# Kernel optimization log

Hardware: AMD Instinct MI355X
Metric: run time of the kernel (lower is better)

## Reference

```python
import jax, jax.numpy as jnp
import numpy as np

N_NODES = 100_000
N_EDGES = 1_600_000
N_GRAPHS = 1_000
NODES_PER_GRAPH = 100
N_NODE_FEATS = 64
DIM_STATE = 32
DIM_OUT = 64
DIM_NODE_EMB = 64
HID = 128
HEADS = 8
BASES = 4


def _lin(key, out_f, in_f, bias=True):
    k1, k2 = jax.random.split(key)
    lim = 1.0 / np.sqrt(in_f)
    w = jax.random.uniform(k1, (out_f, in_f), minval=-lim, maxval=lim, dtype=jnp.float32)
    if not bias:
        return w
    b = jax.random.uniform(k2, (out_f,), minval=-lim, maxval=lim, dtype=jnp.float32)
    return w, b


def setup_inputs() -> dict:
    key = jax.random.key(0)
    ks = jax.random.split(key, 16)
    x = jax.random.normal(ks[0], (N_NODES, N_NODE_FEATS), dtype=jnp.float32)
    edge_index = jax.random.randint(ks[1], (2, N_EDGES), 0, N_NODES, dtype=jnp.int32)
    batch = jnp.arange(N_NODES, dtype=jnp.int32) // NODES_PER_GRAPH  # sorted segment ids
    n_atoms = jnp.full((N_GRAPHS, 1), NODES_PER_GRAPH, dtype=jnp.int32)  # consistent with batch
    z_e = jax.random.normal(ks[2], (N_GRAPHS, DIM_STATE), dtype=jnp.float32)
    nfc_w, nfc_b = _lin(ks[3], HID, N_NODE_FEATS)
    # EGConv: bases Linear(in, (out//heads)*bases, no bias); comb Linear(in, heads*bases); bias (out,)
    gc1_bases_w = _lin(ks[4], (HID // HEADS) * BASES, HID, bias=False)
    gc1_comb_w, gc1_comb_b = _lin(ks[5], HEADS * BASES, HID)
    gc1_bias = jnp.zeros((HID,), jnp.float32)
    gc2_bases_w = _lin(ks[6], (DIM_NODE_EMB // HEADS) * BASES, HID, bias=False)
    gc2_comb_w, gc2_comb_b = _lin(ks[7], HEADS * BASES, HID)
    gc2_bias = jnp.zeros((DIM_NODE_EMB,), jnp.float32)
    attn_w, attn_b = _lin(ks[8], 1, DIM_NODE_EMB + DIM_STATE)
    fcg_w, fcg_b = _lin(ks[9], DIM_OUT, DIM_NODE_EMB)
    fccg_w, fccg_b = _lin(ks[10], DIM_OUT, DIM_NODE_EMB)
    return {"x": x, "edge_index": edge_index, "batch": batch, "n_atoms": n_atoms, "z_e": z_e,
            "nfc_w": nfc_w, "nfc_b": nfc_b,
            "gc1_bases_w": gc1_bases_w, "gc1_comb_w": gc1_comb_w, "gc1_comb_b": gc1_comb_b, "gc1_bias": gc1_bias,
            "gc2_bases_w": gc2_bases_w, "gc2_comb_w": gc2_comb_w, "gc2_comb_b": gc2_comb_b, "gc2_bias": gc2_bias,
            "attn_w": attn_w, "attn_b": attn_b, "fcg_w": fcg_w, "fcg_b": fcg_b, "fccg_w": fccg_w, "fccg_b": fccg_b}


def _egconv(h, src, dst, bases_w, comb_w, comb_b, bias, heads=HEADS, nbases=BASES):
    # PyG EGConv with aggregators=['symnorm'], add_self_loops=True
    n = h.shape[0]
    out_ch = bias.shape[0]
    deg = jnp.ones((n,), h.dtype).at[dst].add(1.0)          # in-degree + self loop
    dis = jax.lax.rsqrt(deg)                                 # deg^-1/2
    b = h @ bases_w.T                                        # [n, nbases*(out_ch//heads)]
    # symnorm aggregation incl. self-loop term dis_i^2 * b_i
    agg = ((dis * dis)[:, None] * b).at[dst].add((dis[src] * dis[dst])[:, None] * b[src])
    w = (h @ comb_w.T + comb_b).reshape(n, heads, nbases)    # [n, H, B]
    agg = agg.reshape(n, nbases, out_ch // heads)            # [n, B, F/H]
    return jnp.einsum('nhb,nbf->nhf', w, agg).reshape(n, out_ch) + bias


def reference(x, edge_index, batch, n_atoms, z_e, nfc_w, nfc_b,
              gc1_bases_w, gc1_comb_w, gc1_comb_b, gc1_bias,
              gc2_bases_w, gc2_comb_w, gc2_comb_b, gc2_bias,
              attn_w, attn_b, fcg_w, fcg_b, fccg_w, fccg_b):
    src, dst = edge_index[0], edge_index[1]
    h = jax.nn.elu(x @ nfc_w.T + nfc_b)
    h = jax.nn.elu(_egconv(h, src, dst, gc1_bases_w, gc1_comb_w, gc1_comb_b, gc1_bias))
    h = jax.nn.elu(_egconv(h, src, dst, gc2_bases_w, gc2_comb_w, gc2_comb_b, gc2_bias))
    h = h / jnp.maximum(jnp.linalg.norm(h, axis=1, keepdims=True), 1e-12)  # L2 normalize
    z_a = jax.ops.segment_sum(h, batch, num_segments=N_GRAPHS) @ fcg_w.T + fcg_b
    z_rep = jnp.repeat(z_e, n_atoms[:, 0], axis=0, total_repeat_length=N_NODES)
    logits = jnp.concatenate([h, z_rep], axis=1) @ attn_w.T + attn_b + 1e-16  # [N,1]
    m = jax.ops.segment_max(logits, batch, num_segments=N_GRAPHS)
    e = jnp.exp(logits - m[batch])
    denom = jax.ops.segment_sum(e, batch, num_segments=N_GRAPHS) + 1e-16
    attns = e / denom[batch]
    z_c = jax.ops.segment_sum(attns * h, batch, num_segments=N_GRAPHS) @ fccg_w.T + fccg_b
    return z_a, z_c, h
```

## Files before the change

### kernel.cpp

```cpp
#include <hip/hip_runtime.h>
#include <hip/hip_bf16.h>
#include <math.h>

#define N_NODES  100000
#define N_EDGES  1600000
#define N_GRAPHS 1000
#define NPG      100
#define NBKT     391
#define BCAP     5120
#define EPB      16384
#define NBE      ((N_EDGES + EPB - 1) / EPB)
#define GBA      ((N_NODES + 63) / 64)

typedef float  f32x4 __attribute__((ext_vector_type(4)));
typedef short  s16x8 __attribute__((ext_vector_type(8)));

__device__ __forceinline__ float elu_f(float x) {
    return x > 0.0f ? x : expm1f(x);
}
__device__ __forceinline__ float bf2f(unsigned int u16) {
    union { unsigned int i; float f; } v; v.i = u16 << 16; return v.f;
}
__device__ __forceinline__ unsigned short f2bf(float f) {
    __hip_bfloat16 h = __float2bfloat16(f);
    return *reinterpret_cast<unsigned short*>(&h);
}
__device__ __forceinline__ s16x8 cvt8(const float4& a, const float4& b) {
    s16x8 o;
    o[0]=(short)f2bf(a.x); o[1]=(short)f2bf(a.y); o[2]=(short)f2bf(a.z); o[3]=(short)f2bf(a.w);
    o[4]=(short)f2bf(b.x); o[5]=(short)f2bf(b.y); o[6]=(short)f2bf(b.z); o[7]=(short)f2bf(b.w);
    return o;
}

__global__ __launch_bounds__(512) void setup_k(
    int* __restrict__ bkt_cur,
    const float* __restrict__ w0, const float* __restrict__ w1c, const float* __restrict__ w1w,
    const float* __restrict__ w2c, const float* __restrict__ w2w, unsigned short* __restrict__ wb)
{
    int t = threadIdx.x;
    if (blockIdx.x == 0 && t < NBKT) bkt_cur[t] = t * BCAP;
    int i = blockIdx.x * 512 + t;
    float v;
    if (i < 8192)       v = w0[i];
    else if (i < 16384) v = w1c[i - 8192];
    else if (i < 20480) v = w1w[i - 16384];
    else if (i < 24576) v = w2c[i - 20480];
    else if (i < 28672) v = w2w[i - 24576];
    else return;
    wb[i] = f2bf(v);
}

__global__ __launch_bounds__(256) void scatterA_k(
    const float* __restrict__ x, const unsigned short* __restrict__ wb,
    const float* __restrict__ b0, const float* __restrict__ bw,
    unsigned short* __restrict__ c1out, float* __restrict__ w1out, int M,
    const int* __restrict__ ei, int* __restrict__ bkt_cur, unsigned int* __restrict__ pairs)
{
    __shared__ union {
        struct { int h[NBKT]; int base[NBKT]; } sc;
        unsigned short hT[64][136];
    } u;

    const int t = threadIdx.x;

    if (blockIdx.x < NBE) {
        const int eb = blockIdx.x;
        int* h = u.sc.h;
        int* base = u.sc.base;
        for (int i = t; i < NBKT; i += 256) h[i] = 0;
        __syncthreads();
        const int4* src4 = (const int4*)ei;
        const int4* dst4 = (const int4*)(ei + N_EDGES);
        int i0 = eb * (EPB / 4);
        for (int i = t; i < EPB / 4; i += 256) {
            int g = i0 + i;
            if (g < N_EDGES / 4) {
                int4 d = dst4[g];
                atomicAdd(&h[d.x >> 8], 1);
                atomicAdd(&h[d.y >> 8], 1);
                atomicAdd(&h[d.z >> 8], 1);
                atomicAdd(&h[d.w >> 8], 1);
            }
        }
        __syncthreads();
        for (int i = t; i < NBKT; i += 256) {
            int c = h[i];
            base[i] = c ? atomicAdd(&bkt_cur[i], c) : 0;
            h[i] = 0;
        }
        __syncthreads();
        for (int i = t; i < EPB / 4; i += 256) {
            int g = i0 + i;
            if (g < N_EDGES / 4) {
                int4 s4 = src4[g];
                int4 d4 = dst4[g];
                int b, r;
                b = d4.x >> 8; r = atomicAdd(&h[b], 1); pairs[base[b] + r] = ((unsigned)s4.x << 8) | (d4.x & 255);
                b = d4.y >> 8; r = atomicAdd(&h[b], 1); pairs[base[b] + r] = ((unsigned)s4.y << 8) | (d4.y & 255);
                b = d4.z >> 8; r = atomicAdd(&h[b], 1); pairs[base[b] + r] = ((unsigned)s4.z << 8) | (d4.z & 255);
                b = d4.w >> 8; r = atomicAdd(&h[b], 1); pairs[base[b] + r] = ((unsigned)s4.w << 8) | (d4.w & 255);
            }
        }
        return;
    }

    const unsigned short* W0b = wb;
    const unsigned short* Wcb = wb + 8192;
    const unsigned short* Wwb = wb + 16384;

    const int wave = t >> 6, lane = t & 63;
    const int lr = lane & 15, lk = lane >> 4;
    const int blockRow = (blockIdx.x - NBE) * 64;

    {
        const int wr = wave >> 1, wc = wave & 1;
        f32x4 acc[2][4];
        #pragma unroll
        for (int rt = 0; rt < 2; ++rt)
            #pragma unroll
            for (int ct = 0; ct < 4; ++ct) acc[rt][ct] = (f32x4){0.f,0.f,0.f,0.f};

        #pragma unroll
        for (int kt = 0; kt < 2; ++kt) {
            const int k0 = kt * 32 + lk * 8;
            s16x8 afr[2];
            #pragma unroll
            for (int rt = 0; rt < 2; ++rt) {
                int r = blockRow + (wr * 2 + rt) * 16 + lr;
                r = (r < M) ? r : (M - 1);
                const float* ap = x + (size_t)r * 64 + k0;
                afr[rt] = cvt8(*(const float4*)ap, *(const float4*)(ap + 4));
            }
            s16x8 bfr[4];
            #pragma unroll
            for (int ct = 0; ct < 4; ++ct) {
                int n = (wc * 4 + ct) * 16 + lr;
                bfr[ct] = *(const s16x8*)(W0b + (size_t)n * 64 + k0);
            }
            #pragma unroll
            for (int rt = 0; rt < 2; ++rt)
                #pragma unroll
                for (int ct = 0; ct < 4; ++ct)
                    acc[rt][ct] = __builtin_amdgcn_mfma_f32_16x16x32_bf16(afr[rt], bfr[ct], acc[rt][ct], 0, 0, 0);
        }
        #pragma unroll
        for (int rt = 0; rt < 2; ++rt) {
            int lmb = (wr * 2 + rt) * 16 + lk * 4;
            #pragma unroll
            for (int j = 0; j < 4; ++j) {
                #pragma unroll
                for (int ct = 0; ct < 4; ++ct) {
                    int n = (wc * 4 + ct) * 16 + lr;
                    u.hT[lmb + j][n] = f2bf(elu_f(acc[rt][ct][j] + b0[n]));
                }
            }
        }
    }
    __syncthreads();

    {
        f32x4 acc[6];
        #pragma unroll
        for (int ct = 0; ct < 6; ++ct) acc[ct] = (f32x4){0.f,0.f,0.f,0.f};
        #pragma unroll
        for (int kt = 0; kt < 4; ++kt) {
            const int k0 = kt * 32 + lk * 8;
            s16x8 af = *(const s16x8*)&u.hT[wave * 16 + lr][k0];
            #pragma unroll
            for (int ct = 0; ct < 6; ++ct) {
                int n = ct * 16 + lr;
                const unsigned short* wp = (n < 64) ? (Wcb + (size_t)n * 128 + k0)
                                                    : (Wwb + (size_t)(n - 64) * 128 + k0);
                acc[ct] = __builtin_amdgcn_mfma_f32_16x16x32_bf16(af, *(const s16x8*)wp, acc[ct], 0, 0, 0);
            }
        }
        int mbase = blockRow + wave * 16 + lk * 4;
        #pragma unroll
        for (int j = 0; j < 4; ++j) {
            int m = mbase + j;
            if (m >= M) continue;
            #pragma unroll
            for (int ct = 0; ct < 6; ++ct) {
                int n = ct * 16 + lr;
                float v = acc[ct][j];
                if (n < 64) c1out[(size_t)m * 64 + n] = f2bf(v);
                else        w1out[(size_t)m * 32 + (n - 64)] = v + bw[n - 64];
            }
        }
    }
}

__global__ __launch_bounds__(256) void bucket_csr_k(const unsigned int* __restrict__ pairs,
                                                    const int* __restrict__ bkt_cur,
                                                    int* __restrict__ starts,
                                                    int* __restrict__ cnt,
                                                    float* __restrict__ dis,
                                                    int* __restrict__ srclist)
{
    __shared__ int s[256];
    __shared__ int cur[256];
    const int b = blockIdx.x, t = threadIdx.x;
    const int lo = b * BCAP;
    const int hi = bkt_cur[b];
    const int n0 = b << 8;
    const int nn = min(256, N_NODES - n0);

    s[t] = 0;
    __syncthreads();
    for (int i = lo + t; i < hi; i += 256) {
        unsigned int p = pairs[i];
        atomicAdd(&s[p & 255], 1);
    }
    __syncthreads();
    int v = s[t];
    __syncthreads();
    s[t] = v;
    __syncthreads();
    #pragma unroll
    for (int off = 1; off < 256; off <<= 1) {
        int u = (t >= off) ? s[t - off] : 0;
        __syncthreads();
        s[t] += u;
        __syncthreads();
    }
    int ex = lo + s[t] - v;
    if (t < nn) {
        starts[n0 + t] = ex;
        cnt[n0 + t] = v;
        dis[n0 + t] = rsqrtf(1.0f + (float)v);
    }
    cur[t] = ex;
    __syncthreads();
    for (int i = lo + t; i < hi; i += 256) {
        unsigned int p = pairs[i];
        int pos = atomicAdd(&cur[p & 255], 1);
        srclist[pos] = (int)(p >> 8);
    }
}

__global__ __launch_bounds__(256) void mgemmL2_k(
    const unsigned short* __restrict__ Ab, const unsigned short* __restrict__ wb,
    const float* __restrict__ bw, const float* __restrict__ dis,
    unsigned short* __restrict__ c2out, float* __restrict__ w2out, int M)
{
    const unsigned short* Wcb = wb + 20480;
    const unsigned short* Wwb = wb + 24576;

    const int t = threadIdx.x;
    const int wave = t >> 6, lane = t & 63;
    const int wr = wave >> 1, wc = wave & 1;
    const int lr = lane & 15, lk = lane >> 4;
    const int blockRow = blockIdx.x * 64;

    f32x4 acc[2][2];
    #pragma unroll
    for (int rt = 0; rt < 2; ++rt)
        #pragma unroll
        for (int ct = 0; ct < 2; ++ct) acc[rt][ct] = (f32x4){0.f,0.f,0.f,0.f};

    #pragma unroll
    for (int kt = 0; kt < 4; ++kt) {
        const int k0 = kt * 32 + lk * 8;
        s16x8 afr[2];
        #pragma unroll
        for (int rt = 0; rt < 2; ++rt) {
            int r = blockRow + (wr * 2 + rt) * 16 + lr;
            r = (r < M) ? r : (M - 1);
            afr[rt] = *(const s16x8*)(Ab + (size_t)r * 128 + k0);
        }
        s16x8 bfr[2];
        #pragma unroll
        for (int ct = 0; ct < 2; ++ct) {
            int n = (wc * 2 + ct) * 16 + lr;
            const unsigned short* wp = (n < 32) ? (Wcb + (size_t)n * 128 + k0)
                                                : (Wwb + (size_t)(n - 32) * 128 + k0);
            bfr[ct] = *(const s16x8*)wp;
        }
        #pragma unroll
        for (int rt = 0; rt < 2; ++rt)
            #pragma unroll
            for (int ct = 0; ct < 2; ++ct)
                acc[rt][ct] = __builtin_amdgcn_mfma_f32_16x16x32_bf16(afr[rt], bfr[ct], acc[rt][ct], 0, 0, 0);
    }

    #pragma unroll
    for (int rt = 0; rt < 2; ++rt) {
        int mbase = blockRow + (wr * 2 + rt) * 16 + lk * 4;
        #pragma unroll
        for (int j = 0; j < 4; ++j) {
            int m = mbase + j;
            if (m >= M) continue;
            float dsc = dis[m];
            #pragma unroll
            for (int ct = 0; ct < 2; ++ct) {
                int n = (wc * 2 + ct) * 16 + lr;
                float v = acc[rt][ct][j];
                if (n < 32) c2out[(size_t)m * 32 + n] = f2bf(dsc * v);
                else        w2out[(size_t)m * 32 + (n - 32)] = v + bw[n - 32];
            }
        }
    }
}

__global__ __launch_bounds__(256) void gather1_k(
    const int* __restrict__ starts, const int* __restrict__ cnt,
    const int* __restrict__ srclist, const unsigned short* __restrict__ c,
    const float* __restrict__ w1, const float* __restrict__ dis,
    const float* __restrict__ bias, unsigned short* __restrict__ h2b)
{
    __shared__ float aggS[4][68];

    const int t = threadIdx.x;
    const int nn   = t >> 6;
    const int lane = t & 63;
    const int q    = lane & 15;
    const int slot = lane >> 4;
    const int n    = blockIdx.x * 4 + nn;

    const int s0 = starts[n];
    const int cn = cnt[n];
    float a0 = 0.f, a1 = 0.f, a2 = 0.f, a3 = 0.f;
    if (slot == 0) {
        float dsn = dis[n];
        uint2 u = *(const uint2*)(c + (size_t)n * 64 + q * 4);
        a0 = dsn * bf2f(u.x & 0xffff); a1 = dsn * bf2f(u.x >> 16);
        a2 = dsn * bf2f(u.y & 0xffff); a3 = dsn * bf2f(u.y >> 16);
    }
    for (int j = slot; j < cn; j += 4) {
        int src = srclist[s0 + j];
        float ds = dis[src];
        uint2 u = *(const uint2*)(c + (size_t)src * 64 + q * 4);
        a0 = fmaf(ds, bf2f(u.x & 0xffff), a0); a1 = fmaf(ds, bf2f(u.x >> 16), a1);
        a2 = fmaf(ds, bf2f(u.y & 0xffff), a2); a3 = fmaf(ds, bf2f(u.y >> 16), a3);
    }
    a0 += __shfl_xor(a0, 16, 64); a0 += __shfl_xor(a0, 32, 64);
    a1 += __shfl_xor(a1, 16, 64); a1 += __shfl_xor(a1, 32, 64);
    a2 += __shfl_xor(a2, 16, 64); a2 += __shfl_xor(a2, 32, 64);
    a3 += __shfl_xor(a3, 16, 64); a3 += __shfl_xor(a3, 32, 64);
    if (slot == 0) {
        aggS[nn][q * 4 + 0] = a0;
        aggS[nn][q * 4 + 1] = a1;
        aggS[nn][q * 4 + 2] = a2;
        aggS[nn][q * 4 + 3] = a3;
    }
    __syncthreads();

    const float dn = dis[n];
    const float* wr = w1 + (size_t)n * 32;
    unsigned short* out = h2b + (size_t)n * 128;
    #pragma unroll
    for (int r = 0; r < 2; ++r) {
        int j = r * 64 + lane;
        int hh = j >> 4, f = j & 15;
        float4 wv = *(const float4*)(wr + hh * 4);
        float s = wv.x * aggS[nn][0 * 16 + f] + wv.y * aggS[nn][1 * 16 + f]
                + wv.z * aggS[nn][2 * 16 + f] + wv.w * aggS[nn][3 * 16 + f];
        out[j] = f2bf(elu_f(s * dn + bias[j]));
    }
}

__global__ __launch_bounds__(256) void gather2_k(
    const int* __restrict__ starts, const int* __restrict__ cnt,
    const int* __restrict__ srclist, const unsigned short* __restrict__ c,
    const float* __restrict__ w2, const float* __restrict__ dis,
    const float* __restrict__ bias, float* __restrict__ hout)
{
    __shared__ float aggS[4][36];

    const int t = threadIdx.x;
    const int nn   = t >> 6;
    const int lane = t & 63;
    const int q    = lane & 15;
    const int slot = lane >> 4;
    const int n    = blockIdx.x * 4 + nn;

    const int s0 = starts[n];
    const int cn = cnt[n];
    float a0 = 0.f, a1 = 0.f;
    if (slot == 0) {
        unsigned int u = *(const unsigned int*)(c + (size_t)n * 32 + q * 2);
        a0 = bf2f(u & 0xffff); a1 = bf2f(u >> 16);
    }
    for (int j = slot; j < cn; j += 4) {
        int src = srclist[s0 + j];
        unsigned int u = *(const unsigned int*)(c + (size_t)src * 32 + q * 2);
        a0 += bf2f(u & 0xffff); a1 += bf2f(u >> 16);
    }
    a0 += __shfl_xor(a0, 16, 64); a0 += __shfl_xor(a0, 32, 64);
    a1 += __shfl_xor(a1, 16, 64); a1 += __shfl_xor(a1, 32, 64);
    if (slot == 0) {
        aggS[nn][q * 2 + 0] = a0;
        aggS[nn][q * 2 + 1] = a1;
    }
    __syncthreads();

    const float dn = dis[n];
    const int hh = lane >> 3, f = lane & 7;
    float4 wv = *(const float4*)(w2 + (size_t)n * 32 + hh * 4);
    float s = wv.x * aggS[nn][0 * 8 + f] + wv.y * aggS[nn][1 * 8 + f]
            + wv.z * aggS[nn][2 * 8 + f] + wv.w * aggS[nn][3 * 8 + f];
    float sv = elu_f(s * dn + bias[lane]);

    float tot = sv * sv;
    #pragma unroll
    for (int o = 1; o < 64; o <<= 1) tot += __shfl_xor(tot, o, 64);
    float inv = 1.0f / fmaxf(sqrtf(tot), 1e-12f);
    hout[(size_t)n * 64 + lane] = sv * inv;
}

__global__ __launch_bounds__(128) void graph_k(const float* __restrict__ h,
                                               const float* __restrict__ z_e,
                                               const float* __restrict__ aw,
                                               const float* __restrict__ ab,
                                               const float* __restrict__ fcgw,
                                               const float* __restrict__ fcgb,
                                               const float* __restrict__ fccgw,
                                               const float* __restrict__ fccgb,
                                               float* __restrict__ z_a,
                                               float* __restrict__ z_c)
{
    __shared__ float Hs[NPG * 64];
    __shared__ float sumh[64], wsh[64], lg[NPG], ex[NPG];
    __shared__ float red[2];
    int g = blockIdx.x, t = threadIdx.x;
    const float* hg = h + (size_t)g * NPG * 64;
    for (int idx = t; idx < NPG * 64; idx += 128) Hs[idx] = hg[idx];
    __syncthreads();

    if (t < 64) {
        float s = 0.0f;
        for (int n = 0; n < NPG; ++n) s += Hs[n * 64 + t];
        sumh[t] = s;
    }
    __syncthreads();

    if (t < 64) {
        float acc = fcgb[t];
        for (int f = 0; f < 64; ++f) acc = fmaf(sumh[f], fcgw[t * 64 + f], acc);
        z_a[(size_t)g * 64 + t] = acc;
    }
    if (t < NPG) {
        float zd = 0.0f;
        for (int q = 0; q < 32; ++q) zd = fmaf(z_e[(size_t)g * 32 + q], aw[64 + q], zd);
        float dot = 0.0f;
        for (int k0 = 0; k0 < 64; ++k0) {
            int k = (k0 + t) & 63;
            dot = fmaf(Hs[t * 64 + k], aw[k], dot);
        }
        lg[t] = dot + zd + ab[0] + 1e-16f;
    }
    __syncthreads();

    if (t < 64) {
        float m = -INFINITY;
        for (int n = t; n < NPG; n += 64) m = fmaxf(m, lg[n]);
        #pragma unroll
        for (int o = 1; o < 64; o <<= 1) m = fmaxf(m, __shfl_xor(m, o, 64));
        if (t == 0) red[0] = m;
    }
    __syncthreads();
    float m = red[0];
    if (t < NPG) ex[t] = expf(lg[t] - m);
    __syncthreads();
    if (t < 64) {
        float s = 0.0f;
        for (int n = t; n < NPG; n += 64) s += ex[n];
        #pragma unroll
        for (int o = 1; o < 64; o <<= 1) s += __shfl_xor(s, o, 64);
        if (t == 0) red[1] = s + 1e-16f;
    }
    __syncthreads();
    float inv_denom = 1.0f / red[1];
    if (t < 64) {
        float a = 0.0f;
        for (int n = 0; n < NPG; ++n) a = fmaf(ex[n], Hs[n * 64 + t], a);
        wsh[t] = a * inv_denom;
    }
    __syncthreads();
    if (t < 64) {
        float acc = fccgb[t];
        for (int f = 0; f < 64; ++f) acc = fmaf(wsh[f], fccgw[t * 64 + f], acc);
        z_c[(size_t)g * 64 + t] = acc;
    }
}

extern "C" void kernel_launch(void* const* d_in, const int* in_sizes, int n_in,
                              void* d_out, int out_size, void* d_ws, size_t ws_size,
                              hipStream_t stream)
{
    const float* x     = (const float*)d_in[0];
    const int*   ei    = (const int*)d_in[1];
    const float* z_e   = (const float*)d_in[4];
    const float* nfc_w = (const float*)d_in[5];
    const float* nfc_b = (const float*)d_in[6];
    const float* g1bw  = (const float*)d_in[7];
    const float* g1cw  = (const float*)d_in[8];
    const float* g1cb  = (const float*)d_in[9];
    const float* g1b   = (const float*)d_in[10];
    const float* g2bw  = (const float*)d_in[11];
    const float* g2cw  = (const float*)d_in[12];
    const float* g2cb  = (const float*)d_in[13];
    const float* g2b   = (const float*)d_in[14];
    const float* aw    = (const float*)d_in[15];
    const float* ab    = (const float*)d_in[16];
    const float* fcgw  = (const float*)d_in[17];
    const float* fcgb  = (const float*)d_in[18];
    const float* fccgw = (const float*)d_in[19];
    const float* fccgb = (const float*)d_in[20];

    float* ws        = (float*)d_ws;
    float* dis       = ws;
    int*   cnt       = (int*)(ws + 102400);
    int*   starts    = cnt + 102400;
    int*   bkt_cur   = starts + 102400;
    int*   srclist   = bkt_cur + 512;
    float* hbuf      = (float*)(srclist + 2002048);
    float* c1f       = hbuf + 6400000;
    float* w1        = c1f + 3200000;
    float* c2f       = w1 + 3200000;
    float* w2        = c2f + 1600000;
    unsigned short* wb = (unsigned short*)(w2 + 3200000);
    unsigned int*  pairs = (unsigned int*)hbuf;
    unsigned short* hb = (unsigned short*)hbuf;
    unsigned short* c1 = (unsigned short*)c1f;
    unsigned short* c2 = (unsigned short*)c2f;

    float* z_a  = (float*)d_out;
    float* z_c  = z_a + (size_t)N_GRAPHS * 64;
    float* hout = z_a + (size_t)2 * N_GRAPHS * 64;

    setup_k<<<57, 512, 0, stream>>>(bkt_cur, nfc_w, g1bw, g1cw, g2bw, g2cw, wb);
    scatterA_k<<<NBE + GBA, 256, 0, stream>>>(x, wb, nfc_b, g1cb, c1, w1, N_NODES,
                                              ei, bkt_cur, pairs);
    bucket_csr_k<<<NBKT, 256, 0, stream>>>(pairs, bkt_cur, starts, cnt, dis, srclist);
    gather1_k<<<N_NODES / 4, 256, 0, stream>>>(starts, cnt, srclist, c1, w1, dis, g1b, hb);
    mgemmL2_k<<<GBA, 256, 0, stream>>>(hb, wb, g2cb, dis, c2, w2, N_NODES);
    gather2_k<<<N_NODES / 4, 256, 0, stream>>>(starts, cnt, srclist, c2, w2, dis, g2b, hout);
    graph_k<<<N_GRAPHS, 128, 0, stream>>>(hout, z_e, aw, ab, fcgw, fcgb, fccgw, fccgb, z_a, z_c);
}
```

Before: 235.6 us.

## Fuse layer-2 projection GEMM into first gather kernel

Removes the separate MFMA GEMM kernel for the second EGConv layer. Each gather1 block now stages the transposed layer-2 weights in shared memory and computes the 64 output columns per node with scalar FMAs. This avoids writing and re-reading the intermediate hidden activations and one kernel launch. In exchange, every block reloads the weight matrix, adds shared memory pressure that can reduce occupancy, and gives up tensor-core math.

```diff
diff --git a/kernel.cpp b/kernel.cpp
--- a/kernel.cpp
+++ b/kernel.cpp
@@ -238,77 +238,17 @@
     }
 }
 
-__global__ __launch_bounds__(256) void mgemmL2_k(
-    const unsigned short* __restrict__ Ab, const unsigned short* __restrict__ wb,
-    const float* __restrict__ bw, const float* __restrict__ dis,
-    unsigned short* __restrict__ c2out, float* __restrict__ w2out, int M)
-{
-    const unsigned short* Wcb = wb + 20480;
-    const unsigned short* Wwb = wb + 24576;
-
-    const int t = threadIdx.x;
-    const int wave = t >> 6, lane = t & 63;
-    const int wr = wave >> 1, wc = wave & 1;
-    const int lr = lane & 15, lk = lane >> 4;
-    const int blockRow = blockIdx.x * 64;
-
-    f32x4 acc[2][2];
-    #pragma unroll
-    for (int rt = 0; rt < 2; ++rt)
-        #pragma unroll
-        for (int ct = 0; ct < 2; ++ct) acc[rt][ct] = (f32x4){0.f,0.f,0.f,0.f};
-
-    #pragma unroll
-    for (int kt = 0; kt < 4; ++kt) {
-        const int k0 = kt * 32 + lk * 8;
-        s16x8 afr[2];
-        #pragma unroll
-        for (int rt = 0; rt < 2; ++rt) {
-            int r = blockRow + (wr * 2 + rt) * 16 + lr;
-            r = (r < M) ? r : (M - 1);
-            afr[rt] = *(const s16x8*)(Ab + (size_t)r * 128 + k0);
-        }
-        s16x8 bfr[2];
-        #pragma unroll
-        for (int ct = 0; ct < 2; ++ct) {
-            int n = (wc * 2 + ct) * 16 + lr;
-            const unsigned short* wp = (n < 32) ? (Wcb + (size_t)n * 128 + k0)
-                                                : (Wwb + (size_t)(n - 32) * 128 + k0);
-            bfr[ct] = *(const s16x8*)wp;
-        }
-        #pragma unroll
-        for (int rt = 0; rt < 2; ++rt)
-            #pragma unroll
-            for (int ct = 0; ct < 2; ++ct)
-                acc[rt][ct] = __builtin_amdgcn_mfma_f32_16x16x32_bf16(afr[rt], bfr[ct], acc[rt][ct], 0, 0, 0);
-    }
-
-    #pragma unroll
-    for (int rt = 0; rt < 2; ++rt) {
-        int mbase = blockRow + (wr * 2 + rt) * 16 + lk * 4;
-        #pragma unroll
-        for (int j = 0; j < 4; ++j) {
-            int m = mbase + j;
-            if (m >= M) continue;
-            float dsc = dis[m];
-            #pragma unroll
-            for (int ct = 0; ct < 2; ++ct) {
-                int n = (wc * 2 + ct) * 16 + lr;
-                float v = acc[rt][ct][j];
-                if (n < 32) c2out[(size_t)m * 32 + n] = f2bf(dsc * v);
-                else        w2out[(size_t)m * 32 + (n - 32)] = v + bw[n - 32];
-            }
-        }
-    }
-}
-
 __global__ __launch_bounds__(256) void gather1_k(
     const int* __restrict__ starts, const int* __restrict__ cnt,
     const int* __restrict__ srclist, const unsigned short* __restrict__ c,
     const float* __restrict__ w1, const float* __restrict__ dis,
-    const float* __restrict__ bias, unsigned short* __restrict__ h2b)
+    const float* __restrict__ bias, const unsigned short* __restrict__ wb,
+    const float* __restrict__ bw2,
+    unsigned short* __restrict__ c2out, float* __restrict__ w2out)
 {
     __shared__ float aggS[4][68];
+    __shared__ float hrowS[4][128];
+    __shared__ unsigned short WTs[128][66];
 
     const int t = threadIdx.x;
     const int nn   = t >> 6;
@@ -316,6 +256,11 @@
     const int q    = lane & 15;
     const int slot = lane >> 4;
     const int n    = blockIdx.x * 4 + nn;
+
+    for (int idx = t; idx < 8192; idx += 256) {
+        int k = idx & 127, o = idx >> 7;
+        WTs[k][o] = wb[(o < 32 ? 20480 + o * 128 : 24576 + (o - 32) * 128) + k];
+    }
 
     const int s0 = starts[n];
     const int cn = cnt[n];
@@ -347,7 +292,6 @@
 
     const float dn = dis[n];
     const float* wr = w1 + (size_t)n * 32;
-    unsigned short* out = h2b + (size_t)n * 128;
     #pragma unroll
     for (int r = 0; r < 2; ++r) {
         int j = r * 64 + lane;
@@ -355,8 +299,16 @@
         float4 wv = *(const float4*)(wr + hh * 4);
         float s = wv.x * aggS[nn][0 * 16 + f] + wv.y * aggS[nn][1 * 16 + f]
                 + wv.z * aggS[nn][2 * 16 + f] + wv.w * aggS[nn][3 * 16 + f];
-        out[j] = f2bf(elu_f(s * dn + bias[j]));
-    }
+        float hv = elu_f(s * dn + bias[j]);
+        hrowS[nn][j] = bf2f(f2bf(hv));
+    }
+
+    float acc = 0.0f;
+    #pragma unroll 8
+    for (int k = 0; k < 128; ++k)
+        acc = fmaf(hrowS[nn][k], bf2f(WTs[k][lane]), acc);
+    if (lane < 32) c2out[(size_t)n * 32 + lane]        = f2bf(dn * acc);
+    else           w2out[(size_t)n * 32 + (lane - 32)] = acc + bw2[lane - 32];
 }
 
 __global__ __launch_bounds__(256) void gather2_k(
@@ -521,7 +473,6 @@
     float* w2        = c2f + 1600000;
     unsigned short* wb = (unsigned short*)(w2 + 3200000);
     unsigned int*  pairs = (unsigned int*)hbuf;
-    unsigned short* hb = (unsigned short*)hbuf;
     unsigned short* c1 = (unsigned short*)c1f;
     unsigned short* c2 = (unsigned short*)c2f;
 
@@ -533,8 +484,8 @@
     scatterA_k<<<NBE + GBA, 256, 0, stream>>>(x, wb, nfc_b, g1cb, c1, w1, N_NODES,
                                               ei, bkt_cur, pairs);
     bucket_csr_k<<<NBKT, 256, 0, stream>>>(pairs, bkt_cur, starts, cnt, dis, srclist);
-    gather1_k<<<N_NODES / 4, 256, 0, stream>>>(starts, cnt, srclist, c1, w1, dis, g1b, hb);
-    mgemmL2_k<<<GBA, 256, 0, stream>>>(hb, wb, g2cb, dis, c2, w2, N_NODES);
+    gather1_k<<<N_NODES / 4, 256, 0, stream>>>(starts, cnt, srclist, c1, w1, dis, g1b,
+                                               wb, g2cb, c2, w2);
     gather2_k<<<N_NODES / 4, 256, 0, stream>>>(starts, cnt, srclist, c2, w2, dis, g2b, hout);
     graph_k<<<N_GRAPHS, 128, 0, stream>>>(hout, z_e, aw, ab, fcgw, fcgb, fccgw, fccgb, z_a, z_c);
 }
```

New measurement: 282.5 us. 1.2x slower.
